# Performance work log

Hardware: AMD Instinct MI355X
Metric: run time of the kernel (lower is better)

The kernel has to match this reference:

```python
import jax, jax.numpy as jnp
import numpy as np

B, S, D_IN, HID, H, OUT = 4, 2048, 1024, 1024, 16, 128
DH = HID // H
SCALE = float(np.sqrt(DH))
ELEV, FLOOR2 = 4, 32


def setup_inputs() -> dict:
    key = jax.random.key(0)
    ks = jax.random.split(key, 12)
    w = lambda k, o, i: jax.random.normal(k, (o, i), dtype=jnp.float32) * 0.02
    b = lambda k, o: jax.random.normal(k, (o,), dtype=jnp.float32) * 0.02
    return {
        "query": jax.random.normal(ks[0], (B, S, D_IN), dtype=jnp.float32),
        "key": jax.random.normal(ks[1], (B, S, D_IN), dtype=jnp.float32),
        "value": jax.random.normal(ks[2], (B, S, D_IN), dtype=jnp.float32),
        "mask": jax.random.randint(ks[3], (B, 1, 1, S), 0, 2, dtype=jnp.int32),
        "wq_w": w(ks[4], HID, D_IN), "wq_b": b(ks[5], HID),
        "wk_w": w(ks[6], HID, D_IN), "wk_b": b(ks[7], HID),
        "wv_w": w(ks[8], HID, D_IN), "wv_b": b(ks[9], HID),
        "fc_w": w(ks[10], OUT, HID), "fc_b": b(ks[11], OUT),
    }


def reference(query, key, value, mask, wq_w, wq_b, wk_w, wk_b, wv_w, wv_b, fc_w, fc_b):
    bsz, seq = query.shape[0], query.shape[1]
    # torch Linear: x @ W.T + b
    split = lambda x: x.reshape(bsz, seq, H, DH).transpose(0, 2, 1, 3)  # (b,h,s,dh)
    Q = split(query @ wq_w.T + wq_b)
    K = split(key @ wk_w.T + wk_b)
    V = split(value @ wv_w.T + wv_b)
    energy = jnp.einsum('bhqd,bhkd->bhqk', Q, K) / SCALE
    energy = jnp.where(mask == 0, jnp.float32(-1e10), energy)
    attn = jax.nn.softmax(energy, axis=-1)  # dropout is identity in eval mode
    x = jnp.einsum('bhqk,bhkd->bhqd', attn, V)
    x = x.transpose(0, 2, 1, 3).reshape(bsz, seq, HID)
    x = x @ fc_w.T + fc_b
    x = x.reshape(-1, ELEV, FLOOR2)  # (b*s, elevator_num, floor_num*2)
    return jax.nn.softmax(x, axis=1)  # nn.Softmax(dim=1)
```

## Files before the change

### kernel.cpp

```cpp
#include <hip/hip_runtime.h>
#include <stdint.h>

#define S_LEN 2048
#define DK 1024
#define NH 16
#define DH 64
#define LOG2E 1.4426950408889634f
#define M_FIX 10.0f

typedef __attribute__((ext_vector_type(8))) short bf16x8;
typedef __attribute__((ext_vector_type(4))) float f32x4;

__device__ __forceinline__ unsigned short f2bf(float f) {
    union { float f; uint32_t u; } v; v.f = f;
    return (unsigned short)((v.u + 0x7fffu + ((v.u >> 16) & 1u)) >> 16);
}

__device__ __forceinline__ float fast_exp2(float x) {
#if __has_builtin(__builtin_amdgcn_exp2f)
    return __builtin_amdgcn_exp2f(x);
#else
    return exp2f(x);
#endif
}

__device__ __forceinline__ uint32_t cvt_pk_bf16(float a, float b) {
    uint32_t r;
    asm("v_cvt_pk_bf16_f32 %0, %1, %2" : "=v"(r) : "v"(a), "v"(b));
    return r;
}

__device__ __forceinline__ void gload_lds16(const void* g, void* l) {
    __builtin_amdgcn_global_load_lds((const __attribute__((address_space(1))) void*)g,
                                     (__attribute__((address_space(3))) void*)l, 16, 0, 0);
}

__global__ __launch_bounds__(256) void cvt3_kernel(
    const float* __restrict__ a0, const float* __restrict__ a1, const float* __restrict__ a2,
    unsigned short* __restrict__ o0, unsigned short* __restrict__ o1, unsigned short* __restrict__ o2,
    int n4)
{
    const float* in = (blockIdx.y == 0) ? a0 : ((blockIdx.y == 1) ? a1 : a2);
    unsigned short* out = (blockIdx.y == 0) ? o0 : ((blockIdx.y == 1) ? o1 : o2);
    const float4* pin = (const float4*)in;
    ushort4* pout = (ushort4*)out;
    int i = blockIdx.x * blockDim.x + threadIdx.x;
    int stride = gridDim.x * blockDim.x;
    for (; i < n4; i += stride) {
        float4 v = pin[i];
        ushort4 o;
        o.x = f2bf(v.x); o.y = f2bf(v.y); o.z = f2bf(v.z); o.w = f2bf(v.w);
        pout[i] = o;
    }
}

__global__ __launch_bounds__(256) void proj_gemm(
    const unsigned short* __restrict__ Xq, const unsigned short* __restrict__ Xk, const unsigned short* __restrict__ Xv,
    const unsigned short* __restrict__ Wq, const unsigned short* __restrict__ Wk, const unsigned short* __restrict__ Wv,
    const float* __restrict__ bq, const float* __restrict__ bk, const float* __restrict__ bv,
    unsigned short* __restrict__ Qh, unsigned short* __restrict__ Kh, unsigned short* __restrict__ Vt)
{
    const int d = blockIdx.x + (blockIdx.y << 3) + (blockIdx.z << 9);
    const int k = d & 7, s = d >> 3;
    const int nn = s & 7;
    const int mz = ((s >> 3) << 3) + k;
    const int m0 = (mz & 63) * 128;
    const int z = mz >> 6;

    const unsigned short* X = (z == 0) ? Xq : ((z == 1) ? Xk : Xv);
    const unsigned short* W = (z == 0) ? Wq : ((z == 1) ? Wk : Wv);
    const float* bias = (z == 0) ? bq : ((z == 1) ? bk : bv);

    const int n0 = nn * 128;
    const int tid = threadIdx.x;
    const int w = tid >> 6;
    const int l = tid & 63;
    const int wm = w >> 1, wn = w & 1;
    const int g = l >> 4, c = l & 15;

    __shared__ __align__(16) unsigned short As[3][128 * 32];
    __shared__ __align__(16) unsigned short Bs[3][128 * 32];

    f32x4 acc[4][4] = {};

    const int srow = l >> 2;
    const int schunk = (((l & 3) - (l >> 3)) & 3) * 8;

    auto stage = [&](int kk, int buf) {
#pragma unroll
        for (int j = 0; j < 2; ++j) {
            int r0 = 32 * w + 16 * j;
            gload_lds16(X + (size_t)(m0 + r0 + srow) * DK + kk + schunk, &As[buf][r0 * 32]);
            gload_lds16(W + (size_t)(n0 + r0 + srow) * DK + kk + schunk, &Bs[buf][r0 * 32]);
        }
    };

    stage(0, 0);
    stage(32, 1);

    int cur = 0;
    for (int step = 0; step < 32; ++step) {
        if (step < 31) asm volatile("s_waitcnt vmcnt(4)" ::: "memory");
        else           asm volatile("s_waitcnt vmcnt(0)" ::: "memory");
        __builtin_amdgcn_s_barrier();
        __builtin_amdgcn_sched_barrier(0);

        if (step < 30) {
            int nb = cur + 2; if (nb >= 3) nb -= 3;
            stage((step + 2) << 5, nb);
        }

        bf16x8 a[4], bb[4];
        const int rchunk = 8 * ((g + (c >> 1)) & 3);
#pragma unroll
        for (int mi = 0; mi < 4; ++mi)
            a[mi] = *(const bf16x8*)&As[cur][(64 * wm + 16 * mi + c) * 32 + rchunk];
#pragma unroll
        for (int nj = 0; nj < 4; ++nj)
            bb[nj] = *(const bf16x8*)&Bs[cur][(64 * wn + 16 * nj + c) * 32 + rchunk];
        __builtin_amdgcn_s_setprio(1);
#pragma unroll
        for (int mi = 0; mi < 4; ++mi)
#pragma unroll
            for (int nj = 0; nj < 4; ++nj)
                acc[mi][nj] = __builtin_amdgcn_mfma_f32_16x16x32_bf16(a[mi], bb[nj], acc[mi][nj], 0, 0, 0);
        __builtin_amdgcn_s_setprio(0);

        ++cur; if (cur == 3) cur = 0;
    }

    const float scale = (z == 0) ? 0.125f : 1.0f;
#pragma unroll
    for (int mi = 0; mi < 4; ++mi) {
#pragma unroll
        for (int nj = 0; nj < 4; ++nj) {
            int col = n0 + 64 * wn + 16 * nj + c;
            float bval = bias[col];
            int h = col >> 6, dh = col & 63;
            int row0 = m0 + 64 * wm + 16 * mi + 4 * g;
            int b = row0 >> 11, ss = row0 & 2047;
            if (z != 2) {
                unsigned short* Out = (z == 0) ? Qh : Kh;
#pragma unroll
                for (int r = 0; r < 4; ++r) {
                    float v = (acc[mi][nj][r] + bval) * scale;
                    Out[((size_t)(b * NH + h) * S_LEN + (ss + r)) * DH + dh] = f2bf(v);
                }
            } else {
                ushort4 o;
                o.x = f2bf(acc[mi][nj][0] + bval);
                o.y = f2bf(acc[mi][nj][1] + bval);
                o.z = f2bf(acc[mi][nj][2] + bval);
                o.w = f2bf(acc[mi][nj][3] + bval);
                int q = (ss >> 2) & 7;
                int newpos = (ss & ~31) + 8 * (q & 3) + 4 * (q >> 2);
                *(ushort4*)&Vt[((size_t)(b * NH + h) * DH + dh) * S_LEN + newpos] = o;
            }
        }
    }
}

__global__ __launch_bounds__(256, 5) void attn_kernel(
    const unsigned short* __restrict__ Qh, const unsigned short* __restrict__ Kh,
    const unsigned short* __restrict__ Vt, const int* __restrict__ maskI,
    unsigned short* __restrict__ O)
{
    const int id = blockIdx.x + (blockIdx.y << 4);
    const int swzid = (id & 7) * 128 + (id >> 3);
    const int q0 = (swzid & 15) * 128;
    const int bh = swzid >> 4;
    const int b = bh >> 4, h = bh & 15;
    const int tid = threadIdx.x, w = tid >> 6, l = tid & 63;
    const int g = l >> 4, c = l & 15;

    __shared__ __align__(16) unsigned short Ks[2][32 * 64];
    __shared__ __align__(16) unsigned short Vs[2][64 * 32];
    __shared__ __align__(16) float mskA[S_LEN];

    bf16x8 qf[2][2];
    const size_t qbase = (size_t)bh * S_LEN + q0 + 32 * w;
#pragma unroll
    for (int mi = 0; mi < 2; ++mi)
#pragma unroll
        for (int k32 = 0; k32 < 2; ++k32)
            qf[mi][k32] = *(const bf16x8*)&Qh[(qbase + 16 * mi + c) * DH + k32 * 32 + 8 * g];

    f32x4 ao[2][4] = {};
    f32x4 ls[2] = {};
    bf16x8 ones;
#pragma unroll
    for (int j = 0; j < 8; ++j) ones[j] = (short)0x3F80;

    const int kswz = ((l & 7) ^ (l >> 3)) * 8;
    const int vrow = l >> 2;
    const int vsrc = (((l & 3) - (l >> 3)) & 3) * 8;

    gload_lds16(Kh + ((size_t)bh * S_LEN + 8 * w + (l >> 3)) * DH + kswz, &Ks[0][w * 512]);
    gload_lds16(Vt + ((size_t)bh * DH + 16 * w + vrow) * S_LEN + vsrc, &Vs[0][w * 512]);
    {
        const int4* mp = (const int4*)(maskI + b * S_LEN);
#pragma unroll
        for (int i = 0; i < 2; ++i) {
            int idx = tid + 256 * i;
            int4 m = mp[idx];
            float4 f;
            f.x = m.x ? (-M_FIX * LOG2E) : -3e38f;
            f.y = m.y ? (-M_FIX * LOG2E) : -3e38f;
            f.z = m.z ? (-M_FIX * LOG2E) : -3e38f;
            f.w = m.w ? (-M_FIX * LOG2E) : -3e38f;
            *(float4*)&mskA[idx * 4] = f;
        }
    }

    for (int t = 0; t < 64; ++t) {
        const int cur = t & 1;
        const int kv0 = t << 5;
        __syncthreads();

        if (t < 63) {
            int kvn = kv0 + 32;
            gload_lds16(Kh + ((size_t)bh * S_LEN + kvn + 8 * w + (l >> 3)) * DH + kswz, &Ks[cur ^ 1][w * 512]);
            gload_lds16(Vt + ((size_t)bh * DH + 16 * w + vrow) * S_LEN + kvn + vsrc, &Vs[cur ^ 1][w * 512]);
        }

        f32x4 sf[2][2] = {};
        __builtin_amdgcn_s_setprio(1);
#pragma unroll
        for (int nj = 0; nj < 2; ++nj) {
            int krow = 16 * nj + c;
#pragma unroll
            for (int k32 = 0; k32 < 2; ++k32) {
                int chunk = (k32 * 4 + g) ^ (krow & 7);
                bf16x8 kf = *(const bf16x8*)&Ks[cur][krow * 64 + chunk * 8];
#pragma unroll
                for (int mi = 0; mi < 2; ++mi)
                    sf[mi][nj] = __builtin_amdgcn_mfma_f32_16x16x32_bf16(kf, qf[mi][k32], sf[mi][nj], 0, 0, 0);
            }
        }
        __builtin_amdgcn_s_setprio(0);

        float4 mk0 = *(const float4*)&mskA[kv0 + 4 * g];
        float4 mk1 = *(const float4*)&mskA[kv0 + 16 + 4 * g];
        bf16x8 pf[2];
#pragma unroll
        for (int mi = 0; mi < 2; ++mi) {
            float e00 = fast_exp2(fmaf(sf[mi][0][0], LOG2E, mk0.x));
            float e01 = fast_exp2(fmaf(sf[mi][0][1], LOG2E, mk0.y));
            float e02 = fast_exp2(fmaf(sf[mi][0][2], LOG2E, mk0.z));
            float e03 = fast_exp2(fmaf(sf[mi][0][3], LOG2E, mk0.w));
            float e10 = fast_exp2(fmaf(sf[mi][1][0], LOG2E, mk1.x));
            float e11 = fast_exp2(fmaf(sf[mi][1][1], LOG2E, mk1.y));
            float e12 = fast_exp2(fmaf(sf[mi][1][2], LOG2E, mk1.z));
            float e13 = fast_exp2(fmaf(sf[mi][1][3], LOG2E, mk1.w));
            union { uint32_t u[4]; bf16x8 v; } pu;
            pu.u[0] = cvt_pk_bf16(e00, e01);
            pu.u[1] = cvt_pk_bf16(e02, e03);
            pu.u[2] = cvt_pk_bf16(e10, e11);
            pu.u[3] = cvt_pk_bf16(e12, e13);
            pf[mi] = pu.v;
        }

        __builtin_amdgcn_s_setprio(1);
#pragma unroll
        for (int nc = 0; nc < 4; ++nc) {
            int row = 16 * nc + c;
            int s16 = (g + (c >> 1)) & 3;
            bf16x8 vf = *(const bf16x8*)&Vs[cur][row * 32 + 8 * s16];
#pragma unroll
            for (int mi = 0; mi < 2; ++mi)
                ao[mi][nc] = __builtin_amdgcn_mfma_f32_16x16x32_bf16(pf[mi], vf, ao[mi][nc], 0, 0, 0);
        }
#pragma unroll
        for (int mi = 0; mi < 2; ++mi)
            ls[mi] = __builtin_amdgcn_mfma_f32_16x16x32_bf16(pf[mi], ones, ls[mi], 0, 0, 0);
        __builtin_amdgcn_s_setprio(0);
    }

#pragma unroll
    for (int mi = 0; mi < 2; ++mi)
#pragma unroll
        for (int r = 0; r < 4; ++r) {
            int s = q0 + 32 * w + 16 * mi + 4 * g + r;
            float inv = 1.0f / ls[mi][r];
#pragma unroll
            for (int nc = 0; nc < 4; ++nc) {
                int dh = 16 * nc + c;
                O[(size_t)(b * S_LEN + s) * 1024 + h * DH + dh] = f2bf(ao[mi][nc][r] * inv);
            }
        }
}

__global__ __launch_bounds__(256) void fc_kernel(
    const unsigned short* __restrict__ O, const unsigned short* __restrict__ Wf,
    const float* __restrict__ bfc, float* __restrict__ out)
{
    const int m0 = blockIdx.x * 64;
    const int tid = threadIdx.x, w = tid >> 6, l = tid & 63;

    __shared__ __align__(16) unsigned short As[64 * 64];
    __shared__ __align__(16) unsigned short Bs[128 * 64];

    f32x4 acc[8] = {};

    for (int k0 = 0; k0 < DK; k0 += 64) {
        __syncthreads();
#pragma unroll
        for (int c = 0; c < 2; ++c) {
            int row = 16 * w + 8 * c + (l >> 3);
            gload_lds16(O + (size_t)(m0 + row) * DK + k0 + (l & 7) * 8, &As[(16 * w + 8 * c) * 64]);
        }
#pragma unroll
        for (int c = 0; c < 4; ++c) {
            int row = 32 * w + 8 * c + (l >> 3);
            gload_lds16(Wf + (size_t)row * DK + k0 + (l & 7) * 8, &Bs[(32 * w + 8 * c) * 64]);
        }
        __syncthreads();
#pragma unroll
        for (int k32 = 0; k32 < 2; ++k32) {
            bf16x8 a = *(const bf16x8*)&As[(16 * w + (l & 15)) * 64 + k32 * 32 + 8 * (l >> 4)];
#pragma unroll
            for (int nj = 0; nj < 8; ++nj) {
                bf16x8 bb = *(const bf16x8*)&Bs[(16 * nj + (l & 15)) * 64 + k32 * 32 + 8 * (l >> 4)];
                acc[nj] = __builtin_amdgcn_mfma_f32_16x16x32_bf16(a, bb, acc[nj], 0, 0, 0);
            }
        }
    }

#pragma unroll
    for (int r = 0; r < 4; ++r) {
        int row = m0 + 16 * w + (l >> 4) * 4 + r;
#pragma unroll
        for (int par = 0; par < 2; ++par) {
            float v[4];
#pragma unroll
            for (int e = 0; e < 4; ++e) {
                int col = 16 * (2 * e + par) + (l & 15);
                v[e] = acc[2 * e + par][r] + bfc[col];
            }
            float mx = fmaxf(fmaxf(v[0], v[1]), fmaxf(v[2], v[3]));
            float ex[4], ssum = 0.f;
#pragma unroll
            for (int e = 0; e < 4; ++e) { ex[e] = fast_exp2((v[e] - mx) * LOG2E); ssum += ex[e]; }
            float inv = 1.0f / ssum;
#pragma unroll
            for (int e = 0; e < 4; ++e) {
                int col = 16 * (2 * e + par) + (l & 15);
                out[(size_t)row * 128 + col] = ex[e] * inv;
            }
        }
    }
}

extern "C" void kernel_launch(void* const* d_in, const int* in_sizes, int n_in,
                              void* d_out, int out_size, void* d_ws, size_t ws_size,
                              hipStream_t stream) {
    (void)in_sizes; (void)n_in; (void)out_size; (void)ws_size;
    const float* q    = (const float*)d_in[0];
    const float* k    = (const float*)d_in[1];
    const float* v    = (const float*)d_in[2];
    const int*   mask = (const int*)d_in[3];
    const float* wq_w = (const float*)d_in[4];
    const float* wq_b = (const float*)d_in[5];
    const float* wk_w = (const float*)d_in[6];
    const float* wk_b = (const float*)d_in[7];
    const float* wv_w = (const float*)d_in[8];
    const float* wv_b = (const float*)d_in[9];
    const float* fc_w = (const float*)d_in[10];
    const float* fc_b = (const float*)d_in[11];

    const size_t NX = (size_t)8192 * 1024;
    const size_t NW = (size_t)1024 * 1024;
    const size_t NF = (size_t)128 * 1024;

    unsigned short* Xq = (unsigned short*)d_ws;
    unsigned short* Xk = Xq + NX;
    unsigned short* Xv = Xk + NX;
    unsigned short* Wq = Xv + NX;
    unsigned short* Wk = Wq + NW;
    unsigned short* Wv = Wk + NW;
    unsigned short* Wf = Wv + NW;
    unsigned short* Qh = Wf + NF;
    unsigned short* Kh = Qh + NX;
    unsigned short* Vt = Kh + NX;
    unsigned short* O  = Xq;

    cvt3_kernel<<<dim3(2048, 3), 256, 0, stream>>>(q, k, v, Xq, Xk, Xv, (int)(NX / 4));
    cvt3_kernel<<<dim3(512, 3), 256, 0, stream>>>(wq_w, wk_w, wv_w, Wq, Wk, Wv, (int)(NW / 4));
    cvt3_kernel<<<dim3(128, 1), 256, 0, stream>>>(fc_w, fc_w, fc_w, Wf, Wf, Wf, (int)(NF / 4));

    proj_gemm<<<dim3(8, 64, 3), 256, 0, stream>>>(Xq, Xk, Xv, Wq, Wk, Wv,
                                                  wq_b, wk_b, wv_b, Qh, Kh, Vt);
    attn_kernel<<<dim3(16, 64), 256, 0, stream>>>(Qh, Kh, Vt, mask, O);
    fc_kernel<<<128, 256, 0, stream>>>(O, Wf, fc_b, (float*)d_out);
}
```

Before: 199.2 us.

## Fuse fp32-to-bf16 activation conversion into projection GEMM A-tile loading

Measured after the change: 215.9 us. +8.4%, slower.

```diff
diff --git a/kernel.cpp b/kernel.cpp
--- a/kernel.cpp
+++ b/kernel.cpp
@@ -54,8 +54,8 @@
     }
 }
 
-__global__ __launch_bounds__(256) void proj_gemm(
-    const unsigned short* __restrict__ Xq, const unsigned short* __restrict__ Xk, const unsigned short* __restrict__ Xv,
+__global__ __launch_bounds__(256, 4) void proj_gemm(
+    const float* __restrict__ Xqf, const float* __restrict__ Xkf, const float* __restrict__ Xvf,
     const unsigned short* __restrict__ Wq, const unsigned short* __restrict__ Wk, const unsigned short* __restrict__ Wv,
     const float* __restrict__ bq, const float* __restrict__ bk, const float* __restrict__ bv,
     unsigned short* __restrict__ Qh, unsigned short* __restrict__ Kh, unsigned short* __restrict__ Vt)
@@ -67,7 +67,7 @@
     const int m0 = (mz & 63) * 128;
     const int z = mz >> 6;
 
-    const unsigned short* X = (z == 0) ? Xq : ((z == 1) ? Xk : Xv);
+    const float* X = (z == 0) ? Xqf : ((z == 1) ? Xkf : Xvf);
     const unsigned short* W = (z == 0) ? Wq : ((z == 1) ? Wk : Wv);
     const float* bias = (z == 0) ? bq : ((z == 1) ? bk : bv);
 
@@ -78,7 +78,7 @@
     const int wm = w >> 1, wn = w & 1;
     const int g = l >> 4, c = l & 15;
 
-    __shared__ __align__(16) unsigned short As[3][128 * 32];
+    __shared__ __align__(16) unsigned short As[2][128 * 32];
     __shared__ __align__(16) unsigned short Bs[3][128 * 32];
 
     f32x4 acc[4][4] = {};
@@ -86,38 +86,62 @@
     const int srow = l >> 2;
     const int schunk = (((l & 3) - (l >> 3)) & 3) * 8;
 
-    auto stage = [&](int kk, int buf) {
+    const int arow8 = l >> 3;
+    const int ap = l & 7;
+
+    auto stageW = [&](int kk, int buf) {
 #pragma unroll
         for (int j = 0; j < 2; ++j) {
             int r0 = 32 * w + 16 * j;
-            gload_lds16(X + (size_t)(m0 + r0 + srow) * DK + kk + schunk, &As[buf][r0 * 32]);
             gload_lds16(W + (size_t)(n0 + r0 + srow) * DK + kk + schunk, &Bs[buf][r0 * 32]);
         }
     };
-
-    stage(0, 0);
-    stage(32, 1);
-
-    int cur = 0;
+    float4 areg[4];
+    auto loadA = [&](int kk) {
+#pragma unroll
+        for (int it = 0; it < 4; ++it) {
+            int row = 32 * w + 8 * it + arow8;
+            areg[it] = *(const float4*)&X[(size_t)(m0 + row) * DK + kk + 4 * ap];
+        }
+    };
+    auto writeA = [&](int buf) {
+#pragma unroll
+        for (int it = 0; it < 4; ++it) {
+            int row = 32 * w + 8 * it + arow8;
+            uint2 pw;
+            pw.x = cvt_pk_bf16(areg[it].x, areg[it].y);
+            pw.y = cvt_pk_bf16(areg[it].z, areg[it].w);
+            int slot = ((ap >> 1) + (row >> 1)) & 3;
+            *(uint2*)&As[buf][row * 32 + slot * 8 + (ap & 1) * 4] = pw;
+        }
+    };
+
+    loadA(0);
+    stageW(0, 0);
+    stageW(32, 1);
+    writeA(0);
+    loadA(32);
+    asm volatile("s_waitcnt vmcnt(6)" ::: "memory");
+    asm volatile("s_waitcnt lgkmcnt(0)" ::: "memory");
+    __builtin_amdgcn_s_barrier();
+    __builtin_amdgcn_sched_barrier(0);
+
+    int curA = 0, curB = 0;
     for (int step = 0; step < 32; ++step) {
-        if (step < 31) asm volatile("s_waitcnt vmcnt(4)" ::: "memory");
-        else           asm volatile("s_waitcnt vmcnt(0)" ::: "memory");
-        __builtin_amdgcn_s_barrier();
-        __builtin_amdgcn_sched_barrier(0);
-
-        if (step < 30) {
-            int nb = cur + 2; if (nb >= 3) nb -= 3;
-            stage((step + 2) << 5, nb);
-        }
-
         bf16x8 a[4], bb[4];
         const int rchunk = 8 * ((g + (c >> 1)) & 3);
 #pragma unroll
         for (int mi = 0; mi < 4; ++mi)
-            a[mi] = *(const bf16x8*)&As[cur][(64 * wm + 16 * mi + c) * 32 + rchunk];
+            a[mi] = *(const bf16x8*)&As[curA][(64 * wm + 16 * mi + c) * 32 + rchunk];
 #pragma unroll
         for (int nj = 0; nj < 4; ++nj)
-            bb[nj] = *(const bf16x8*)&Bs[cur][(64 * wn + 16 * nj + c) * 32 + rchunk];
+            bb[nj] = *(const bf16x8*)&Bs[curB][(64 * wn + 16 * nj + c) * 32 + rchunk];
+
+        if (step < 30) {
+            int nb = curB + 2; if (nb >= 3) nb -= 3;
+            stageW((step + 2) << 5, nb);
+        }
+
         __builtin_amdgcn_s_setprio(1);
 #pragma unroll
         for (int mi = 0; mi < 4; ++mi)
@@ -126,7 +150,15 @@
                 acc[mi][nj] = __builtin_amdgcn_mfma_f32_16x16x32_bf16(a[mi], bb[nj], acc[mi][nj], 0, 0, 0);
         __builtin_amdgcn_s_setprio(0);
 
-        ++cur; if (cur == 3) cur = 0;
+        if (step < 31) {
+            writeA(curA ^ 1);
+            if (step < 30) loadA((step + 2) << 5);
+        }
+
+        asm volatile("s_waitcnt lgkmcnt(0)" ::: "memory");
+        __builtin_amdgcn_s_barrier();
+        __builtin_amdgcn_sched_barrier(0);
+        curA ^= 1; ++curB; if (curB == 3) curB = 0;
     }
 
     const float scale = (z == 0) ? 0.125f : 1.0f;
@@ -384,11 +416,10 @@
     unsigned short* Vt = Kh + NX;
     unsigned short* O  = Xq;
 
-    cvt3_kernel<<<dim3(2048, 3), 256, 0, stream>>>(q, k, v, Xq, Xk, Xv, (int)(NX / 4));
     cvt3_kernel<<<dim3(512, 3), 256, 0, stream>>>(wq_w, wk_w, wv_w, Wq, Wk, Wv, (int)(NW / 4));
     cvt3_kernel<<<dim3(128, 1), 256, 0, stream>>>(fc_w, fc_w, fc_w, Wf, Wf, Wf, (int)(NF / 4));
 
-    proj_gemm<<<dim3(8, 64, 3), 256, 0, stream>>>(Xq, Xk, Xv, Wq, Wk, Wv,
+    proj_gemm<<<dim3(8, 64, 3), 256, 0, stream>>>(q, k, v, Wq, Wk, Wv,
                                                   wq_b, wk_b, wv_b, Qh, Kh, Vt);
     attn_kernel<<<dim3(16, 64), 256, 0, stream>>>(Qh, Kh, Vt, mask, O);
     fc_kernel<<<128, 256, 0, stream>>>(O, Wf, fc_b, (float*)d_out);
```

## Fuse fp32-to-bf16 activation conversion into projection GEMM loads

Applied to the files above, without the earlier changes.

New measurement: 203.8 us. 1.02x slower.

```diff
diff --git a/kernel.cpp b/kernel.cpp
--- a/kernel.cpp
+++ b/kernel.cpp
@@ -55,7 +55,7 @@
 }
 
 __global__ __launch_bounds__(256) void proj_gemm(
-    const unsigned short* __restrict__ Xq, const unsigned short* __restrict__ Xk, const unsigned short* __restrict__ Xv,
+    const float* __restrict__ Xqf, const float* __restrict__ Xkf, const float* __restrict__ Xvf,
     const unsigned short* __restrict__ Wq, const unsigned short* __restrict__ Wk, const unsigned short* __restrict__ Wv,
     const float* __restrict__ bq, const float* __restrict__ bk, const float* __restrict__ bv,
     unsigned short* __restrict__ Qh, unsigned short* __restrict__ Kh, unsigned short* __restrict__ Vt)
@@ -67,7 +67,7 @@
     const int m0 = (mz & 63) * 128;
     const int z = mz >> 6;
 
-    const unsigned short* X = (z == 0) ? Xq : ((z == 1) ? Xk : Xv);
+    const float* X = (z == 0) ? Xqf : ((z == 1) ? Xkf : Xvf);
     const unsigned short* W = (z == 0) ? Wq : ((z == 1) ? Wk : Wv);
     const float* bias = (z == 0) ? bq : ((z == 1) ? bk : bv);
 
@@ -78,19 +78,24 @@
     const int wm = w >> 1, wn = w & 1;
     const int g = l >> 4, c = l & 15;
 
-    __shared__ __align__(16) unsigned short As[3][128 * 32];
+    __shared__ __align__(16) float          Asf[3][128 * 32];
     __shared__ __align__(16) unsigned short Bs[3][128 * 32];
 
     f32x4 acc[4][4] = {};
 
     const int srow = l >> 2;
     const int schunk = (((l & 3) - (l >> 3)) & 3) * 8;
+    const int asrc = 8 * ((((l & 7) >> 1) - (l >> 4)) & 3) + 4 * (l & 1);
 
     auto stage = [&](int kk, int buf) {
+#pragma unroll
+        for (int j = 0; j < 4; ++j) {
+            int row = 32 * w + 8 * j;
+            gload_lds16(X + (size_t)(m0 + row + (l >> 3)) * DK + kk + asrc, &Asf[buf][row * 32]);
+        }
 #pragma unroll
         for (int j = 0; j < 2; ++j) {
             int r0 = 32 * w + 16 * j;
-            gload_lds16(X + (size_t)(m0 + r0 + srow) * DK + kk + schunk, &As[buf][r0 * 32]);
             gload_lds16(W + (size_t)(n0 + r0 + srow) * DK + kk + schunk, &Bs[buf][r0 * 32]);
         }
     };
@@ -100,7 +105,7 @@
 
     int cur = 0;
     for (int step = 0; step < 32; ++step) {
-        if (step < 31) asm volatile("s_waitcnt vmcnt(4)" ::: "memory");
+        if (step < 31) asm volatile("s_waitcnt vmcnt(6)" ::: "memory");
         else           asm volatile("s_waitcnt vmcnt(0)" ::: "memory");
         __builtin_amdgcn_s_barrier();
         __builtin_amdgcn_sched_barrier(0);
@@ -111,13 +116,22 @@
         }
 
         bf16x8 a[4], bb[4];
-        const int rchunk = 8 * ((g + (c >> 1)) & 3);
-#pragma unroll
-        for (int mi = 0; mi < 4; ++mi)
-            a[mi] = *(const bf16x8*)&As[cur][(64 * wm + 16 * mi + c) * 32 + rchunk];
+        const int rslot = (g + (c >> 1)) & 3;
+#pragma unroll
+        for (int mi = 0; mi < 4; ++mi) {
+            int row = 64 * wm + 16 * mi + c;
+            f32x4 lo = *(const f32x4*)&Asf[cur][row * 32 + rslot * 8];
+            f32x4 hi = *(const f32x4*)&Asf[cur][row * 32 + rslot * 8 + 4];
+            union { uint32_t u[4]; bf16x8 v; } au;
+            au.u[0] = cvt_pk_bf16(lo[0], lo[1]);
+            au.u[1] = cvt_pk_bf16(lo[2], lo[3]);
+            au.u[2] = cvt_pk_bf16(hi[0], hi[1]);
+            au.u[3] = cvt_pk_bf16(hi[2], hi[3]);
+            a[mi] = au.v;
+        }
 #pragma unroll
         for (int nj = 0; nj < 4; ++nj)
-            bb[nj] = *(const bf16x8*)&Bs[cur][(64 * wn + 16 * nj + c) * 32 + rchunk];
+            bb[nj] = *(const bf16x8*)&Bs[cur][(64 * wn + 16 * nj + c) * 32 + 8 * rslot];
         __builtin_amdgcn_s_setprio(1);
 #pragma unroll
         for (int mi = 0; mi < 4; ++mi)
@@ -384,11 +398,10 @@
     unsigned short* Vt = Kh + NX;
     unsigned short* O  = Xq;
 
-    cvt3_kernel<<<dim3(2048, 3), 256, 0, stream>>>(q, k, v, Xq, Xk, Xv, (int)(NX / 4));
     cvt3_kernel<<<dim3(512, 3), 256, 0, stream>>>(wq_w, wk_w, wv_w, Wq, Wk, Wv, (int)(NW / 4));
     cvt3_kernel<<<dim3(128, 1), 256, 0, stream>>>(fc_w, fc_w, fc_w, Wf, Wf, Wf, (int)(NF / 4));
 
-    proj_gemm<<<dim3(8, 64, 3), 256, 0, stream>>>(Xq, Xk, Xv, Wq, Wk, Wv,
+    proj_gemm<<<dim3(8, 64, 3), 256, 0, stream>>>(q, k, v, Wq, Wk, Wv,
                                                   wq_b, wk_b, wv_b, Qh, Kh, Vt);
     attn_kernel<<<dim3(16, 64), 256, 0, stream>>>(Qh, Kh, Vt, mask, O);
     fc_kernel<<<128, 256, 0, stream>>>(O, Wf, fc_b, (float*)d_out);
```

## Triple-buffer fc GEMM loads with async LDS prefetch and merge weight conversions

Applied to the files above, without the earlier changes.

Result: faster. 195.2 us (-2.0%).

```diff
diff --git a/kernel.cpp b/kernel.cpp
--- a/kernel.cpp
+++ b/kernel.cpp
@@ -54,6 +54,29 @@
     }
 }
 
+__global__ __launch_bounds__(256) void cvt4_kernel(
+    const float* __restrict__ a0, const float* __restrict__ a1,
+    const float* __restrict__ a2, const float* __restrict__ a3,
+    unsigned short* __restrict__ o0, unsigned short* __restrict__ o1,
+    unsigned short* __restrict__ o2, unsigned short* __restrict__ o3,
+    int n4_012, int n4_3)
+{
+    const int y = blockIdx.y;
+    const float* in = (y == 0) ? a0 : ((y == 1) ? a1 : ((y == 2) ? a2 : a3));
+    unsigned short* out = (y == 0) ? o0 : ((y == 1) ? o1 : ((y == 2) ? o2 : o3));
+    const int n4 = (y == 3) ? n4_3 : n4_012;
+    const float4* pin = (const float4*)in;
+    ushort4* pout = (ushort4*)out;
+    int i = blockIdx.x * blockDim.x + threadIdx.x;
+    int stride = gridDim.x * blockDim.x;
+    for (; i < n4; i += stride) {
+        float4 v = pin[i];
+        ushort4 o;
+        o.x = f2bf(v.x); o.y = f2bf(v.y); o.z = f2bf(v.z); o.w = f2bf(v.w);
+        pout[i] = o;
+    }
+}
+
 __global__ __launch_bounds__(256) void proj_gemm(
     const unsigned short* __restrict__ Xq, const unsigned short* __restrict__ Xk, const unsigned short* __restrict__ Xv,
     const unsigned short* __restrict__ Wq, const unsigned short* __restrict__ Wk, const unsigned short* __restrict__ Wv,
@@ -296,34 +319,53 @@
 {
     const int m0 = blockIdx.x * 64;
     const int tid = threadIdx.x, w = tid >> 6, l = tid & 63;
-
-    __shared__ __align__(16) unsigned short As[64 * 64];
-    __shared__ __align__(16) unsigned short Bs[128 * 64];
+    const int g = l >> 4, c = l & 15;
+
+    __shared__ __align__(16) unsigned short As[3][64 * 32];
+    __shared__ __align__(16) unsigned short Bs[3][128 * 32];
 
     f32x4 acc[8] = {};
 
-    for (int k0 = 0; k0 < DK; k0 += 64) {
-        __syncthreads();
-#pragma unroll
-        for (int c = 0; c < 2; ++c) {
-            int row = 16 * w + 8 * c + (l >> 3);
-            gload_lds16(O + (size_t)(m0 + row) * DK + k0 + (l & 7) * 8, &As[(16 * w + 8 * c) * 64]);
-        }
-#pragma unroll
-        for (int c = 0; c < 4; ++c) {
-            int row = 32 * w + 8 * c + (l >> 3);
-            gload_lds16(Wf + (size_t)row * DK + k0 + (l & 7) * 8, &Bs[(32 * w + 8 * c) * 64]);
-        }
-        __syncthreads();
-#pragma unroll
-        for (int k32 = 0; k32 < 2; ++k32) {
-            bf16x8 a = *(const bf16x8*)&As[(16 * w + (l & 15)) * 64 + k32 * 32 + 8 * (l >> 4)];
-#pragma unroll
-            for (int nj = 0; nj < 8; ++nj) {
-                bf16x8 bb = *(const bf16x8*)&Bs[(16 * nj + (l & 15)) * 64 + k32 * 32 + 8 * (l >> 4)];
-                acc[nj] = __builtin_amdgcn_mfma_f32_16x16x32_bf16(a, bb, acc[nj], 0, 0, 0);
-            }
-        }
+    const int srow = l >> 2;
+    const int schunk = (((l & 3) - (l >> 3)) & 3) * 8;
+
+    auto stage = [&](int kk, int buf) {
+        gload_lds16(O + (size_t)(m0 + 16 * w + srow) * DK + kk + schunk, &As[buf][16 * w * 32]);
+#pragma unroll
+        for (int j = 0; j < 2; ++j) {
+            int r0 = 32 * w + 16 * j;
+            gload_lds16(Wf + (size_t)(r0 + srow) * DK + kk + schunk, &Bs[buf][r0 * 32]);
+        }
+    };
+
+    stage(0, 0);
+    stage(32, 1);
+
+    int cur = 0;
+    for (int step = 0; step < 32; ++step) {
+        if (step < 31) asm volatile("s_waitcnt vmcnt(3)" ::: "memory");
+        else           asm volatile("s_waitcnt vmcnt(0)" ::: "memory");
+        __builtin_amdgcn_s_barrier();
+        __builtin_amdgcn_sched_barrier(0);
+
+        if (step < 30) {
+            int nb = cur + 2; if (nb >= 3) nb -= 3;
+            stage((step + 2) << 5, nb);
+        }
+
+        const int rchunk = 8 * ((g + (c >> 1)) & 3);
+        bf16x8 a = *(const bf16x8*)&As[cur][(16 * w + c) * 32 + rchunk];
+        bf16x8 bb[8];
+#pragma unroll
+        for (int nj = 0; nj < 8; ++nj)
+            bb[nj] = *(const bf16x8*)&Bs[cur][(16 * nj + c) * 32 + rchunk];
+        __builtin_amdgcn_s_setprio(1);
+#pragma unroll
+        for (int nj = 0; nj < 8; ++nj)
+            acc[nj] = __builtin_amdgcn_mfma_f32_16x16x32_bf16(a, bb[nj], acc[nj], 0, 0, 0);
+        __builtin_amdgcn_s_setprio(0);
+
+        ++cur; if (cur == 3) cur = 0;
     }
 
 #pragma unroll
@@ -385,8 +427,9 @@
     unsigned short* O  = Xq;
 
     cvt3_kernel<<<dim3(2048, 3), 256, 0, stream>>>(q, k, v, Xq, Xk, Xv, (int)(NX / 4));
-    cvt3_kernel<<<dim3(512, 3), 256, 0, stream>>>(wq_w, wk_w, wv_w, Wq, Wk, Wv, (int)(NW / 4));
-    cvt3_kernel<<<dim3(128, 1), 256, 0, stream>>>(fc_w, fc_w, fc_w, Wf, Wf, Wf, (int)(NF / 4));
+    cvt4_kernel<<<dim3(512, 4), 256, 0, stream>>>(wq_w, wk_w, wv_w, fc_w,
+                                                  Wq, Wk, Wv, Wf,
+                                                  (int)(NW / 4), (int)(NF / 4));
 
     proj_gemm<<<dim3(8, 64, 3), 256, 0, stream>>>(Xq, Xk, Xv, Wq, Wk, Wv,
                                                   wq_b, wk_b, wv_b, Qh, Kh, Vt);
```
